# Kernel optimization log

Hardware: AMD Instinct MI355X
Metric: run time of the kernel (lower is better)

## Reference

```python
import jax, jax.numpy as jnp
import numpy as np

B, T, D = 256, 200, 32          # batch, time steps, input_size
H, PH, PREP = 512, 256, 16      # hidden_size, p_hidden, prep_hidden
COV, COVH, CLFH = 32, 128, 64   # cov_size, cov_hidden, classification_hidden
DT = 0.05                       # euler step size


def setup_inputs() -> dict:
    key = jax.random.key(0)
    ks = jax.random.split(key, 32)
    n = lambda k, shape, s=0.02: (s * jax.random.normal(k, shape)).astype(jnp.float32)
    inp = {}
    inp["cov"] = jax.random.normal(ks[0], (B, COV), dtype=jnp.float32)
    inp["X"] = jax.random.normal(ks[1], (T, B, D), dtype=jnp.float32)
    inp["M"] = (jax.random.uniform(ks[2], (T, B, D)) < 0.3).astype(jnp.float32)
    # covariates_mapping: Linear(COV,COVH) -> ReLU -> Linear(COVH,H) -> Tanh
    inp["Wc1"] = n(ks[3], (COVH, COV), 0.1); inp["bc1"] = jnp.full((COVH,), 0.05, jnp.float32)
    inp["Wc2"] = n(ks[4], (H, COVH), 0.1);   inp["bc2"] = jnp.full((H,), 0.05, jnp.float32)
    # GRUODECell: three bias-free Linear(H,H)
    inp["Whr"] = n(ks[5], (H, H), 0.05)
    inp["Whz"] = n(ks[6], (H, H), 0.05)
    inp["Whh"] = n(ks[7], (H, H), 0.05)
    # log_normal_dist: Linear(H,PH) -> ReLU -> Linear(PH, 2D)
    inp["Wp1"] = n(ks[8], (PH, H), 0.05);  inp["bp1"] = jnp.full((PH,), 0.05, jnp.float32)
    inp["Wp2"] = n(ks[9], (2 * D, PH), 0.05); inp["bp2"] = jnp.full((2 * D,), 0.05, jnp.float32)
    # GRUObsCell prep params
    std = np.sqrt(2.0 / (4 + PREP))
    inp["w_prep"] = (std * jax.random.normal(ks[10], (D, 4, PREP))).astype(jnp.float32)
    inp["bias_prep"] = jnp.full((D, PREP), 0.1, jnp.float32)
    # torch GRUCell(PREP*D, H): gates ordered (r, z, n)
    inp["W_ih"] = n(ks[11], (3 * H, PREP * D), 0.05)
    inp["W_hh"] = n(ks[12], (3 * H, H), 0.05)
    inp["b_ih"] = jnp.zeros((3 * H,), jnp.float32)
    inp["b_hh"] = jnp.zeros((3 * H,), jnp.float32)
    # classifier: Linear(H,CLFH) -> ReLU -> Linear(CLFH,1)
    inp["Wclf1"] = n(ks[13], (CLFH, H), 0.05); inp["bclf1"] = jnp.full((CLFH,), 0.05, jnp.float32)
    inp["Wclf2"] = n(ks[14], (1, CLFH), 0.05); inp["bclf2"] = jnp.full((1,), 0.05, jnp.float32)
    return inp


def reference(cov, X, M, Wc1, bc1, Wc2, bc2, Whr, Whz, Whh, Wp1, bp1, Wp2, bp2,
              w_prep, bias_prep, W_ih, W_hh, b_ih, b_hh, Wclf1, bclf1, Wclf2, bclf2):
    # initial hidden state from covariates
    h0 = jnp.tanh(jax.nn.relu(cov @ Wc1.T + bc1) @ Wc2.T + bc2)  # [B,H]

    def step(h, inp):
        Xt, Mt = inp  # [B,D], [B,D]
        # autonomous GRU-ODE euler step (impute=False -> zero input x)
        r = jax.nn.sigmoid(h @ Whr.T)
        z = jax.nn.sigmoid(h @ Whz.T)
        u = jnp.tanh((r * h) @ Whh.T)
        h = h + DT * (1.0 - z) * (u - h)
        # log-normal observation distribution from hidden state
        p = jax.nn.relu(h @ Wp1.T + bp1) @ Wp2.T + bp2  # [B,2D]
        mean, logvar = jnp.split(p, 2, axis=1)
        sigma = jnp.exp(0.5 * logvar)
        err = (Xt - mean) / sigma
        # per-feature preprocessing: [B,D,4] x [D,4,PREP] -> [B,D,PREP]
        stacked = jnp.stack([Xt, mean, logvar, err], axis=2)
        gi = jax.nn.relu(jnp.einsum('bdf,dfp->bdp', stacked, w_prep) + bias_prep)
        gi = (gi * Mt[:, :, None]).reshape(Xt.shape[0], -1)  # [B, D*PREP]
        # torch GRUCell update (gates r,z,n)
        gx = gi @ W_ih.T + b_ih
        gh = h @ W_hh.T + b_hh
        xr, xz, xn = jnp.split(gx, 3, axis=1)
        hr, hz, hn = jnp.split(gh, 3, axis=1)
        rg = jax.nn.sigmoid(xr + hr)
        zg = jax.nn.sigmoid(xz + hz)
        ng = jnp.tanh(xn + rg * hn)
        h_new = (1.0 - zg) * ng + zg * h
        # scatter-style update: only rows with at least one observation (i_obs)
        obs = (jnp.sum(Mt, axis=1) > 0.0)[:, None]
        h = jnp.where(obs, h_new, h)
        return h, h

    _, h_path = jax.lax.scan(step, h0, (X, M))  # [T,B,H]
    preds = jax.nn.relu(h_path @ Wclf1.T + bclf1) @ Wclf2.T + bclf2  # [T,B,1]
    return preds
```

## Files before the change

### kernel.cpp

```cpp
#include <hip/hip_runtime.h>
#include <hip/hip_bf16.h>

constexpr int Bn = 256, Tn = 200, Dn = 32, Hn = 512, PHn = 256, PREPn = 16;
constexpr int COVn = 32, COVHn = 128, CLFHn = 64;
constexpr float DTc = 0.05f;
constexpr int NT = 512;

constexpr int CSTR = 32;
constexpr int NLINES = 64;

typedef _Float16 h2v __attribute__((ext_vector_type(2)));
typedef _Float16 f16x8 __attribute__((ext_vector_type(8)));
typedef float f32x4 __attribute__((ext_vector_type(4)));

constexpr int PK_WP1   = 0;
constexpr int PK_WP2   = 131072;
constexpr int PK_WCLF1 = 147456;
constexpr int PK_TOTAL = 180224;

constexpr size_t WS_ACT = 393216;
constexpr size_t WS_OBS = 4587520;
constexpr size_t WS_BAR = 4591616;

__device__ __forceinline__ float sigmoidf(float x) { return 1.0f / (1.0f + __expf(-x)); }

__device__ __forceinline__ float fdot2(unsigned w, unsigned v, float acc) {
#if __has_builtin(__builtin_amdgcn_fdot2)
  return __builtin_amdgcn_fdot2(__builtin_bit_cast(h2v, w),
                                __builtin_bit_cast(h2v, v), acc, false);
#else
  h2v a = __builtin_bit_cast(h2v, w), b = __builtin_bit_cast(h2v, v);
  return acc + (float)a.x * (float)b.x + (float)a.y * (float)b.y;
#endif
}
__device__ __forceinline__ float dotq(uint4 w, uint4 h, float acc) {
  acc = fdot2(w.x, h.x, acc); acc = fdot2(w.y, h.y, acc);
  acc = fdot2(w.z, h.z, acc); acc = fdot2(w.w, h.w, acc);
  return acc;
}
__device__ __forceinline__ unsigned pack2(float a, float b) {
  h2v h; h.x = (_Float16)a; h.y = (_Float16)b;
  return __builtin_bit_cast(unsigned, h);
}

__device__ __forceinline__ void cohS(unsigned long long* p, unsigned long long v) {
  __hip_atomic_store(p, v, __ATOMIC_RELAXED, __HIP_MEMORY_SCOPE_SYSTEM);
}
__device__ __forceinline__ void cohSf(float* p, float v) {
  __hip_atomic_store(p, v, __ATOMIC_RELAXED, __HIP_MEMORY_SCOPE_SYSTEM);
}

__device__ __forceinline__ void bar_arrive(unsigned* ctrs, int rg) {
  __syncthreads();
  if (threadIdx.x == 0)
    __hip_atomic_fetch_add(&ctrs[rg * CSTR], 1u,
                           __ATOMIC_RELAXED, __HIP_MEMORY_SCOPE_AGENT);
}
__device__ __forceinline__ void bar_wait(unsigned* ctrs, int rg, unsigned& ep) {
  ep += 1;
  const unsigned target = ep * 64u;
  if (threadIdx.x == 0) {
    const unsigned* myc = &ctrs[rg * CSTR];
    while (__hip_atomic_load(myc, __ATOMIC_RELAXED, __HIP_MEMORY_SCOPE_AGENT) < target)
      __builtin_amdgcn_s_sleep(1);
  }
  __syncthreads();
}

struct PrepArgs { const float *Wp1, *Wp2, *Wclf1; _Float16* dst; unsigned* bar; };

__global__ void prep_pack_kernel(PrepArgs a) {
  const int idx = blockIdx.x * 256 + threadIdx.x;
  if (idx < NLINES * CSTR) a.bar[idx] = 0u;
  if (idx >= PK_TOTAL) return;
  int off, N, K; const float* src;
  if      (idx < PK_WP2)   { off = PK_WP1;   N = 256; K = 512; src = a.Wp1; }
  else if (idx < PK_WCLF1) { off = PK_WP2;   N = 64;  K = 256; src = a.Wp2; }
  else                     { off = PK_WCLF1; N = 64;  K = 512; src = a.Wclf1; }
  const int li = idx - off, e = li & 7, t2 = li >> 3, j = t2 % N, k8 = t2 / N;
  a.dst[idx] = (_Float16)src[(size_t)j * K + k8 * 8 + e];
}

struct CoopArgs {
  const float *cov, *X, *M;
  const float *Wc1, *bc1, *Wc2, *bc2;
  const float *Whr, *Whz, *Whh;
  const float *bp1, *bp2;
  const float *w_prep, *bias_prep;
  const float *W_ih, *W_hh, *b_ih, *b_hh;
  const float *bclf1, *Wclf2, *bclf2;
  const uint4 *Wp1Q, *Wp2Q, *Wclf1Q;
  char* act;
  float* obs;
  unsigned* bar;
  float* out;
};

__global__ __launch_bounds__(NT)
void gruode_coop(CoopArgs a) {
  const int bid = blockIdx.x, tid = threadIdx.x;
  const int cg = bid >> 2, rg = bid & 3;
  const int g = rg * 64 + cg;
  const int c_loc = tid >> 6, r_loc = tid & 63;
  const int c = cg * 8 + c_loc;
  const int lane = tid & 63, wv = tid >> 6;
  const int mt = wv & 3, kh = wv >> 2;
  const int pp4 = wv >> 2;
  const int rgofs = rg * 64;

  __shared__ __align__(16) uint4 Wrz16[64 * 17];
  __shared__ __align__(16) uint4 Wxrz16[64 * 17];
  __shared__ __align__(16) uint4 Whrz16[64 * 17];
  __shared__ __align__(16) uint4 Whh8[64 * 9];
  __shared__ __align__(16) uint4 Wxn8[64 * 9];
  __shared__ __align__(16) uint4 Whn8[64 * 9];
  __shared__ __align__(16) uint4 stageQ[64 * 64];
  __shared__ float redQ[2][64][17];
  __shared__ __align__(16) uint4 hrowQ[64];
  __shared__ __align__(16) uint4 qrowQ[32];
  __shared__ __align__(8)  _Float16 outH[512];
  __shared__ __align__(8)  _Float16 giH[512];
  __shared__ float bp1L[PHn], bp2L[2 * Dn], pL[2 * Dn];
  __shared__ float xrowL[Dn], mrowL[Dn];
  __shared__ float bclfL[CLFHn], wclf2L[CLFHn], bgL[48];
  __shared__ float obsL[64];

  unsigned long long* outU = (unsigned long long*)outH;
  unsigned long long* giU  = (unsigned long long*)giH;

  auto slabp = [&](int arr, int buf) -> uint4* {
    return (uint4*)(a.act + ((size_t)(arr * 4 + buf) << 18));
  };

  float hfull;
  {
    float* covF = (float*)redQ;
    float* midF = (float*)stageQ;
    for (int i = tid; i < 64 * 32; i += NT)
      covF[i] = a.cov[(size_t)rgofs * COVn + i];
    __syncthreads();
    for (int i = tid; i < 64 * 128; i += NT) {
      const int rr = i >> 7, m = i & 127;
      float acc = a.bc1[m];
      #pragma unroll 8
      for (int k = 0; k < COVn; ++k) acc += covF[rr * 32 + k] * a.Wc1[m * COVn + k];
      midF[i] = fmaxf(acc, 0.0f);
    }
    __syncthreads();
    {
      float acc = a.bc2[c];
      const float* w2 = a.Wc2 + (size_t)c * COVHn;
      #pragma unroll 4
      for (int k = 0; k < COVHn; ++k) acc += midF[r_loc * 128 + k] * w2[k];
      hfull = tanhf(acc);
      outH[r_loc * 8 + c_loc] = (_Float16)hfull;
    }
    __syncthreads();
    unsigned long long* hA3u = (unsigned long long*)slabp(0, 3);
    const size_t oub0 = (size_t)(cg * 256 + rgofs) * 2;
    if (tid < 128) cohS(&hA3u[oub0 + tid], outU[tid]);
    __syncthreads();
  }

  for (int nfo = tid; nfo < 4608; nfo += NT) {
    int li; const float* srow; uint4* dst; int phys;
    if (nfo < 3072) {
      li = nfo & 1023; const int seg = nfo >> 10;
      const int n = li >> 6, q = li & 63;
      const int col = cg * 8 + (n & 7);
      if (seg == 0)      { srow = (n < 8 ? a.Whr : a.Whz) + (size_t)col * Hn; dst = Wrz16; }
      else if (seg == 1) { srow = a.W_ih + (size_t)((n < 8 ? 0 : Hn) + col) * Hn; dst = Wxrz16; }
      else               { srow = a.W_hh + (size_t)((n < 8 ? 0 : Hn) + col) * Hn; dst = Whrz16; }
      phys = q * 17 + n;
      const float* s8 = srow + q * 8;
      uint4 u;
      u.x = pack2(s8[0], s8[1]); u.y = pack2(s8[2], s8[3]);
      u.z = pack2(s8[4], s8[5]); u.w = pack2(s8[6], s8[7]);
      dst[phys] = u;
    } else {
      li = (nfo - 3072) & 511; const int seg = (nfo - 3072) >> 9;
      const int n = li >> 6, q = li & 63;
      const int col = cg * 8 + n;
      if (seg == 0)      { srow = a.Whh + (size_t)col * Hn; dst = Whh8; }
      else if (seg == 1) { srow = a.W_ih + (size_t)(2 * Hn + col) * Hn; dst = Wxn8; }
      else               { srow = a.W_hh + (size_t)(2 * Hn + col) * Hn; dst = Whn8; }
      phys = q * 9 + n;
      const float* s8 = srow + q * 8;
      uint4 u;
      u.x = pack2(s8[0], s8[1]); u.y = pack2(s8[2], s8[3]);
      u.z = pack2(s8[4], s8[5]); u.w = pack2(s8[6], s8[7]);
      dst[phys] = u;
    }
  }
  if (tid < PHn)    bp1L[tid] = a.bp1[tid];
  if (tid < 2 * Dn) bp2L[tid] = a.bp2[tid];
  if (tid < CLFHn)  { bclfL[tid] = a.bclf1[tid]; wclf2L[tid] = a.Wclf2[tid]; }
  if (tid < 48) {
    const int cl = tid / 6, rem = tid % 6, gate = rem >> 1, s = rem & 1;
    const int j = gate * Hn + cg * 8 + cl;
    bgL[tid] = s ? a.b_hh[j] : a.b_ih[j];
  }
  if (tid >= 64 && tid < 96)        xrowL[tid - 64] = a.X[(size_t)g * Dn + (tid - 64)];
  else if (tid >= 96 && tid < 128)  mrowL[tid - 96] = a.M[(size_t)g * Dn + (tid - 96)];
  const float bclf2r = a.bclf2[0];

  unsigned ep = 0;
  bar_arrive(a.bar, rg); bar_wait(a.bar, rg, ep);

  float zz = 0.f, hbc = 0.f;
  const size_t oub = (size_t)(cg * 256 + rgofs) * 2;

  auto stage_fill = [&](const uint4* A) {
    #pragma unroll
    for (int i = 0; i < 8; ++i) {
      const int idx = tid + i * NT;
      stageQ[idx] = A[(size_t)(idx >> 6) * 256 + rgofs + (idx & 63)];
    }
  };

  auto ldA = [&](int ks) -> f16x8 {
    return __builtin_bit_cast(f16x8,
        stageQ[(4 * ks + (lane >> 4)) * 64 + mt * 16 + (lane & 15)]);
  };
  auto mma_wide = [&](const uint4* Bw) -> f32x4 {
    f32x4 acc = {0.f, 0.f, 0.f, 0.f};
    const int n = lane & 15, l4 = lane >> 4;
    #pragma unroll
    for (int i = 0; i < 8; ++i) {
      const int ks = kh * 8 + i;
      const f16x8 bv = __builtin_bit_cast(f16x8, Bw[(ks * 4 + l4) * 17 + n]);
      acc = __builtin_amdgcn_mfma_f32_16x16x32_f16(ldA(ks), bv, acc, 0, 0, 0);
    }
    return acc;
  };
  auto mma_half = [&](const uint4* Bw) -> f32x4 {
    f32x4 acc = {0.f, 0.f, 0.f, 0.f};
    const int n = lane & 15, l4 = lane >> 4;
    #pragma unroll
    for (int i = 0; i < 8; ++i) {
      const int ks = kh * 8 + i;
      uint4 ub = {0u, 0u, 0u, 0u};
      if (n < 8) ub = Bw[(ks * 4 + l4) * 9 + n];
      acc = __builtin_amdgcn_mfma_f32_16x16x32_f16(ldA(ks), __builtin_bit_cast(f16x8, ub),
                                                   acc, 0, 0, 0);
    }
    return acc;
  };
  auto redw = [&](f32x4 acc) {
    const int col = lane & 15, r0 = mt * 16 + ((lane >> 4) << 2);
    #pragma unroll
    for (int j = 0; j < 4; ++j) redQ[kh][r0 + j][col] = acc[j];
  };
  auto mma_p4 = [&](const uint4* Bw16, const uint4* Bw9) {
    f32x4 acc = {0.f, 0.f, 0.f, 0.f};
    const int n = lane & 15, l4 = lane >> 4;
    #pragma unroll
    for (int ks = 0; ks < 16; ++ks) {
      uint4 ub = {0u, 0u, 0u, 0u};
      if (pp4 == 0)      ub = Bw16[(ks * 4 + l4) * 17 + n];
      else if (n < 8)    ub = Bw9[(ks * 4 + l4) * 9 + n];
      acc = __builtin_amdgcn_mfma_f32_16x16x32_f16(ldA(ks), __builtin_bit_cast(f16x8, ub),
                                                   acc, 0, 0, 0);
    }
    const int col = lane & 15, r0 = mt * 16 + ((lane >> 4) << 2);
    #pragma unroll
    for (int j = 0; j < 4; ++j) redQ[pp4][r0 + j][col] = acc[j];
  };

  auto do_clf = [&](const uint4* hAbase, int tout) {
    if (tid < CLFHn) {
      hrowQ[tid] = hAbase[(size_t)tid * 256 + g];
      float acc = bclfL[tid];
      #pragma unroll 8
      for (int q = 0; q < Hn / 8; ++q) acc = dotq(a.Wclf1Q[q * CLFHn + tid], hrowQ[q], acc);
      float cc = fmaxf(acc, 0.0f) * wclf2L[tid];
      #pragma unroll
      for (int o = 32; o; o >>= 1) cc += __shfl_down(cc, o, 64);
      if (tid == 0) a.out[tout * Bn + g] = cc + bclf2r;
    }
  };

  for (int t = 0; t < Tn; ++t) {
    if ((t & 3) == 0) __builtin_amdgcn_fence(__ATOMIC_ACQUIRE, "agent");

    const int bs = t & 3, bp = (t + 3) & 3;
    const uint4* hA_prev = slabp(0, bp);
    uint4* rh_cur = slabp(1, bs);
    uint4* hB_cur = slabp(2, bs);
    uint4* gi_cur = slabp(3, bs);
    uint4* hA_cur = slabp(0, bs);
    float* obs_cur = a.obs + bs * 256;

    stage_fill(hA_prev);
    __syncthreads();
    redw(mma_wide(Wrz16));
    __syncthreads();
    {
      const float sr = redQ[0][r_loc][c_loc]     + redQ[1][r_loc][c_loc];
      const float sz = redQ[0][r_loc][c_loc + 8] + redQ[1][r_loc][c_loc + 8];
      const float rr = sigmoidf(sr);
      zz = sigmoidf(sz);
      outH[r_loc * 8 + c_loc] = (_Float16)(rr * hfull);
    }
    __syncthreads();
    if (tid < 128) cohS(((unsigned long long*)rh_cur) + oub + tid, outU[tid]);
    bar_arrive(a.bar, rg);
    if (t > 0) do_clf(hA_prev, t - 1);
    bar_wait(a.bar, rg, ep);

    stage_fill(rh_cur);
    __syncthreads();
    redw(mma_half(Whh8));
    __syncthreads();
    {
      const float su = redQ[0][r_loc][c_loc] + redQ[1][r_loc][c_loc];
      const float u = tanhf(su);
      hbc = hfull + DTc * (1.0f - zz) * (u - hfull);
      outH[r_loc * 8 + c_loc] = (_Float16)hbc;
    }
    __syncthreads();
    if (tid < 128) cohS(((unsigned long long*)hB_cur) + oub + tid, outU[tid]);
    bar_arrive(a.bar, rg);
    bar_wait(a.bar, rg, ep);

    if (tid < 64) hrowQ[tid] = hB_cur[(size_t)tid * 256 + g];
    __syncthreads();
    if (tid < PHn) {
      float a0 = bp1L[tid], a1 = 0.f;
      #pragma unroll 8
      for (int q = 0; q < Hn / 8; q += 2) {
        a0 = dotq(a.Wp1Q[q * PHn + tid], hrowQ[q], a0);
        a1 = dotq(a.Wp1Q[(q + 1) * PHn + tid], hrowQ[q + 1], a1);
      }
      ((_Float16*)qrowQ)[tid] = (_Float16)fmaxf(a0 + a1, 0.0f);
    }
    __syncthreads();
    if (tid < 2 * Dn) {
      float acc = bp2L[tid];
      #pragma unroll 4
      for (int q = 0; q < PHn / 8; ++q)
        acc = dotq(a.Wp2Q[q * (2 * Dn) + tid], qrowQ[q], acc);
      pL[tid] = acc;
    }
    __syncthreads();
    {
      const int d = tid >> 4, pp = tid & 15;
      const float xv   = xrowL[d];
      const float mean = pL[d];
      const float logv = pL[Dn + d];
      const float err  = (xv - mean) * __expf(-0.5f * logv);
      float acc = a.bias_prep[d * PREPn + pp];
      acc += xv   * a.w_prep[(d * 4 + 0) * PREPn + pp];
      acc += mean * a.w_prep[(d * 4 + 1) * PREPn + pp];
      acc += logv * a.w_prep[(d * 4 + 2) * PREPn + pp];
      acc += err  * a.w_prep[(d * 4 + 3) * PREPn + pp];
      giH[tid] = (_Float16)(fmaxf(acc, 0.0f) * mrowL[d]);
      if (tid < 32) {
        const unsigned long long bb = __ballot(mrowL[tid] > 0.0f);
        if (tid == 0) cohSf(&obs_cur[g], bb ? 1.0f : 0.0f);
      }
    }
    __syncthreads();
    if (tid < 128)
      cohS(((unsigned long long*)gi_cur) + (size_t)(tid >> 1) * 512 + g * 2 + (tid & 1), giU[tid]);
    bar_arrive(a.bar, rg);

    stage_fill(hB_cur);
    __syncthreads();
    mma_p4(Whrz16, Whn8);
    __syncthreads();
    const float hr = redQ[0][r_loc][c_loc];
    const float hz = redQ[0][r_loc][c_loc + 8];
    const float hn = redQ[1][r_loc][c_loc];
    bar_wait(a.bar, rg, ep);

    stage_fill(gi_cur);
    if (tid < 64) obsL[tid] = obs_cur[rgofs + tid];
    __syncthreads();
    mma_p4(Wxrz16, Wxn8);
    __syncthreads();
    {
      const float xr = redQ[0][r_loc][c_loc];
      const float xz = redQ[0][r_loc][c_loc + 8];
      const float xn = redQ[1][r_loc][c_loc];
      const float rgg = sigmoidf(xr + hr + bgL[c_loc * 6 + 0] + bgL[c_loc * 6 + 1]);
      const float zgg = sigmoidf(xz + hz + bgL[c_loc * 6 + 2] + bgL[c_loc * 6 + 3]);
      const float ng  = tanhf(xn + bgL[c_loc * 6 + 4] + rgg * (hn + bgL[c_loc * 6 + 5]));
      hfull = (obsL[r_loc] > 0.0f) ? ((1.0f - zgg) * ng + zgg * hbc) : hbc;
      outH[r_loc * 8 + c_loc] = (_Float16)hfull;
    }
    __syncthreads();
    if (tid < 128) cohS(((unsigned long long*)hA_cur) + oub + tid, outU[tid]);
    bar_arrive(a.bar, rg);
    if (t + 1 < Tn) {
      if (tid >= 64 && tid < 96)        xrowL[tid - 64] = a.X[((size_t)(t + 1) * Bn + g) * Dn + (tid - 64)];
      else if (tid >= 96 && tid < 128)  mrowL[tid - 96] = a.M[((size_t)(t + 1) * Bn + g) * Dn + (tid - 96)];
    }
    bar_wait(a.bar, rg, ep);
  }

  do_clf(slabp(0, (Tn - 1) & 3), Tn - 1);
}

extern "C" void kernel_launch(void* const* d_in, const int* in_sizes, int n_in,
                              void* d_out, int out_size, void* d_ws, size_t ws_size,
                              hipStream_t stream) {
  char* ws = (char*)d_ws;

  CoopArgs a;
  a.cov  = (const float*)d_in[0];
  a.X    = (const float*)d_in[1];
  a.M    = (const float*)d_in[2];
  a.Wc1  = (const float*)d_in[3];  a.bc1 = (const float*)d_in[4];
  a.Wc2  = (const float*)d_in[5];  a.bc2 = (const float*)d_in[6];
  a.Whr  = (const float*)d_in[7];  a.Whz = (const float*)d_in[8];  a.Whh = (const float*)d_in[9];
  const float* Wp1 = (const float*)d_in[10]; a.bp1 = (const float*)d_in[11];
  const float* Wp2 = (const float*)d_in[12]; a.bp2 = (const float*)d_in[13];
  a.w_prep = (const float*)d_in[14]; a.bias_prep = (const float*)d_in[15];
  a.W_ih = (const float*)d_in[16]; a.W_hh = (const float*)d_in[17];
  a.b_ih = (const float*)d_in[18]; a.b_hh = (const float*)d_in[19];
  const float* Wclf1 = (const float*)d_in[20]; a.bclf1 = (const float*)d_in[21];
  a.Wclf2 = (const float*)d_in[22]; a.bclf2 = (const float*)d_in[23];

  _Float16* pk = (_Float16*)ws;
  a.Wp1Q   = (const uint4*)(pk + PK_WP1);
  a.Wp2Q   = (const uint4*)(pk + PK_WP2);
  a.Wclf1Q = (const uint4*)(pk + PK_WCLF1);
  a.act = ws + WS_ACT;
  a.obs = (float*)(ws + WS_OBS);
  a.bar = (unsigned*)(ws + WS_BAR);
  a.out = (float*)d_out;

  PrepArgs p;
  p.Wp1 = Wp1; p.Wp2 = Wp2; p.Wclf1 = Wclf1;
  p.dst = pk; p.bar = a.bar;
  prep_pack_kernel<<<(PK_TOTAL + 255) / 256, 256, 0, stream>>>(p);
  gruode_coop<<<Bn, NT, 0, stream>>>(a);
}
```

Baseline: 5.083 ms.

## Compute obs-cell prep redundantly per block with MFMA, dropping one grid barrier

```diff
diff --git a/kernel.cpp b/kernel.cpp
--- a/kernel.cpp
+++ b/kernel.cpp
@@ -7,7 +7,6 @@
 constexpr int NT = 512;
 
 constexpr int CSTR = 32;
-constexpr int NLINES = 64;
 
 typedef _Float16 h2v __attribute__((ext_vector_type(2)));
 typedef _Float16 f16x8 __attribute__((ext_vector_type(8)));
@@ -16,11 +15,11 @@
 constexpr int PK_WP1   = 0;
 constexpr int PK_WP2   = 131072;
 constexpr int PK_WCLF1 = 147456;
-constexpr int PK_TOTAL = 180224;
-
-constexpr size_t WS_ACT = 393216;
-constexpr size_t WS_OBS = 4587520;
-constexpr size_t WS_BAR = 4591616;
+constexpr int PK_WIH   = 180224;
+constexpr int PK_TOTAL = 966656;
+
+constexpr size_t WS_ACT = 1933312;
+constexpr size_t WS_BAR = 4292608;
 
 __device__ __forceinline__ float sigmoidf(float x) { return 1.0f / (1.0f + __expf(-x)); }
 
@@ -44,9 +43,6 @@
 }
 
 __device__ __forceinline__ void cohS(unsigned long long* p, unsigned long long v) {
-  __hip_atomic_store(p, v, __ATOMIC_RELAXED, __HIP_MEMORY_SCOPE_SYSTEM);
-}
-__device__ __forceinline__ void cohSf(float* p, float v) {
   __hip_atomic_store(p, v, __ATOMIC_RELAXED, __HIP_MEMORY_SCOPE_SYSTEM);
 }
 
@@ -67,18 +63,27 @@
   __syncthreads();
 }
 
-struct PrepArgs { const float *Wp1, *Wp2, *Wclf1; _Float16* dst; unsigned* bar; };
+struct PrepArgs { const float *Wp1, *Wp2, *Wclf1, *W_ih; _Float16* dst; unsigned* bar; };
 
 __global__ void prep_pack_kernel(PrepArgs a) {
   const int idx = blockIdx.x * 256 + threadIdx.x;
-  if (idx < NLINES * CSTR) a.bar[idx] = 0u;
+  if (idx < 4 * CSTR) a.bar[idx] = 0u;
   if (idx >= PK_TOTAL) return;
-  int off, N, K; const float* src;
-  if      (idx < PK_WP2)   { off = PK_WP1;   N = 256; K = 512; src = a.Wp1; }
-  else if (idx < PK_WCLF1) { off = PK_WP2;   N = 64;  K = 256; src = a.Wp2; }
-  else                     { off = PK_WCLF1; N = 64;  K = 512; src = a.Wclf1; }
-  const int li = idx - off, e = li & 7, t2 = li >> 3, j = t2 % N, k8 = t2 / N;
-  a.dst[idx] = (_Float16)src[(size_t)j * K + k8 * 8 + e];
+  if (idx < PK_WIH) {
+    int off, N, K; const float* src;
+    if      (idx < PK_WP2)   { off = PK_WP1;   N = 256; K = 512; src = a.Wp1; }
+    else if (idx < PK_WCLF1) { off = PK_WP2;   N = 64;  K = 256; src = a.Wp2; }
+    else                     { off = PK_WCLF1; N = 64;  K = 512; src = a.Wclf1; }
+    const int li = idx - off, e = li & 7, t2 = li >> 3, j = t2 % N, k8 = t2 / N;
+    a.dst[idx] = (_Float16)src[(size_t)j * K + k8 * 8 + e];
+  } else {
+    const int li = idx - PK_WIH;
+    const int e = li & 7, t2 = li >> 3;
+    const int col = t2 % 24, u = t2 / 24;
+    const int k8 = u & 63, cg = u >> 6;
+    const int gate = col >> 3;
+    a.dst[idx] = (_Float16)a.W_ih[(size_t)(gate * Hn + cg * 8 + (col & 7)) * Hn + k8 * 8 + e];
+  }
 }
 
 struct CoopArgs {
@@ -89,9 +94,8 @@
   const float *w_prep, *bias_prep;
   const float *W_ih, *W_hh, *b_ih, *b_hh;
   const float *bclf1, *Wclf2, *bclf2;
-  const uint4 *Wp1Q, *Wp2Q, *Wclf1Q;
+  const uint4 *Wp1Q, *Wp2Q, *Wclf1Q, *WihQ;
   char* act;
-  float* obs;
   unsigned* bar;
   float* out;
 };
@@ -104,32 +108,31 @@
   const int c_loc = tid >> 6, r_loc = tid & 63;
   const int c = cg * 8 + c_loc;
   const int lane = tid & 63, wv = tid >> 6;
-  const int mt = wv & 3, kh = wv >> 2;
-  const int pp4 = wv >> 2;
+  const int mtw = wv & 3, kh = wv >> 2;
+  const int n16 = lane & 15, l4 = lane >> 4;
   const int rgofs = rg * 64;
 
-  __shared__ __align__(16) uint4 Wrz16[64 * 17];
-  __shared__ __align__(16) uint4 Wxrz16[64 * 17];
-  __shared__ __align__(16) uint4 Whrz16[64 * 17];
-  __shared__ __align__(16) uint4 Whh8[64 * 9];
-  __shared__ __align__(16) uint4 Wxn8[64 * 9];
-  __shared__ __align__(16) uint4 Whn8[64 * 9];
+  __shared__ __align__(16) uint4 Wrz16L[64 * 16];
+  __shared__ __align__(16) uint4 Whrz16L[64 * 16];
+  __shared__ __align__(16) uint4 Whh8L[64 * 8];
+  __shared__ __align__(16) uint4 Whn8L[64 * 8];
   __shared__ __align__(16) uint4 stageQ[64 * 64];
   __shared__ float redQ[2][64][17];
-  __shared__ __align__(16) uint4 hrowQ[64];
-  __shared__ __align__(16) uint4 qrowQ[32];
-  __shared__ __align__(8)  _Float16 outH[512];
-  __shared__ __align__(8)  _Float16 giH[512];
-  __shared__ float bp1L[PHn], bp2L[2 * Dn], pL[2 * Dn];
-  __shared__ float xrowL[Dn], mrowL[Dn];
+  __shared__ _Float16 pT[64][66];
+  __shared__ float xrowT[32][64];
+  __shared__ unsigned mmaskL[64];
+  __shared__ float wprepL[Dn * 4 * PREPn];
+  __shared__ float bprepL[Dn * PREPn];
+  __shared__ float bp1L[PHn], bp2L[2 * Dn];
   __shared__ float bclfL[CLFHn], wclf2L[CLFHn], bgL[48];
-  __shared__ float obsL[64];
-
-  unsigned long long* outU = (unsigned long long*)outH;
-  unsigned long long* giU  = (unsigned long long*)giH;
+  __shared__ __align__(16) uint4 sh64[64];
+
+  _Float16* stageH = (_Float16*)stageQ;
+  unsigned long long* outU = (unsigned long long*)sh64;
+  _Float16* outH = (_Float16*)sh64;
 
   auto slabp = [&](int arr, int buf) -> uint4* {
-    return (uint4*)(a.act + ((size_t)(arr * 4 + buf) << 18));
+    return (uint4*)(a.act + ((size_t)(arr * 3 + buf) << 18));
   };
 
   float hfull;
@@ -153,45 +156,44 @@
       #pragma unroll 4
       for (int k = 0; k < COVHn; ++k) acc += midF[r_loc * 128 + k] * w2[k];
       hfull = tanhf(acc);
-      outH[r_loc * 8 + c_loc] = (_Float16)hfull;
-    }
-    __syncthreads();
-    unsigned long long* hA3u = (unsigned long long*)slabp(0, 3);
+    }
+    __syncthreads();
+    outH[r_loc * 8 + c_loc] = (_Float16)hfull;
+    __syncthreads();
+    unsigned long long* hA2u = (unsigned long long*)slabp(0, 2);
     const size_t oub0 = (size_t)(cg * 256 + rgofs) * 2;
-    if (tid < 128) cohS(&hA3u[oub0 + tid], outU[tid]);
+    if (tid < 128) cohS(&hA2u[oub0 + tid], outU[tid]);
     __syncthreads();
   }
 
-  for (int nfo = tid; nfo < 4608; nfo += NT) {
-    int li; const float* srow; uint4* dst; int phys;
-    if (nfo < 3072) {
-      li = nfo & 1023; const int seg = nfo >> 10;
-      const int n = li >> 6, q = li & 63;
-      const int col = cg * 8 + (n & 7);
-      if (seg == 0)      { srow = (n < 8 ? a.Whr : a.Whz) + (size_t)col * Hn; dst = Wrz16; }
-      else if (seg == 1) { srow = a.W_ih + (size_t)((n < 8 ? 0 : Hn) + col) * Hn; dst = Wxrz16; }
-      else               { srow = a.W_hh + (size_t)((n < 8 ? 0 : Hn) + col) * Hn; dst = Whrz16; }
-      phys = q * 17 + n;
-      const float* s8 = srow + q * 8;
-      uint4 u;
-      u.x = pack2(s8[0], s8[1]); u.y = pack2(s8[2], s8[3]);
-      u.z = pack2(s8[4], s8[5]); u.w = pack2(s8[6], s8[7]);
-      dst[phys] = u;
+  for (int nfo = tid; nfo < 3072; nfo += NT) {
+    const float* srow; uint4* dst; int q, phys;
+    if (nfo < 1024) {
+      q = nfo & 63; const int n = nfo >> 6;
+      srow = (n < 8 ? a.Whr + (size_t)(cg * 8 + n) * Hn
+                    : a.Whz + (size_t)(cg * 8 + n - 8) * Hn);
+      dst = Wrz16L; phys = q * 16 + n;
+    } else if (nfo < 2048) {
+      const int li = nfo - 1024; q = li & 63; const int n = li >> 6;
+      srow = a.W_hh + (size_t)((n < 8 ? 0 : Hn) + cg * 8 + (n & 7)) * Hn;
+      dst = Whrz16L; phys = q * 16 + n;
+    } else if (nfo < 2560) {
+      const int li = nfo - 2048; q = li & 63; const int n = li >> 6;
+      srow = a.Whh + (size_t)(cg * 8 + n) * Hn;
+      dst = Whh8L; phys = q * 8 + n;
     } else {
-      li = (nfo - 3072) & 511; const int seg = (nfo - 3072) >> 9;
-      const int n = li >> 6, q = li & 63;
-      const int col = cg * 8 + n;
-      if (seg == 0)      { srow = a.Whh + (size_t)col * Hn; dst = Whh8; }
-      else if (seg == 1) { srow = a.W_ih + (size_t)(2 * Hn + col) * Hn; dst = Wxn8; }
-      else               { srow = a.W_hh + (size_t)(2 * Hn + col) * Hn; dst = Whn8; }
-      phys = q * 9 + n;
-      const float* s8 = srow + q * 8;
-      uint4 u;
-      u.x = pack2(s8[0], s8[1]); u.y = pack2(s8[2], s8[3]);
-      u.z = pack2(s8[4], s8[5]); u.w = pack2(s8[6], s8[7]);
-      dst[phys] = u;
-    }
+      const int li = nfo - 2560; q = li & 63; const int n = li >> 6;
+      srow = a.W_hh + (size_t)(2 * Hn + cg * 8 + n) * Hn;
+      dst = Whn8L; phys = q * 8 + n;
+    }
+    const float* s8 = srow + q * 8;
+    uint4 u;
+    u.x = pack2(s8[0], s8[1]); u.y = pack2(s8[2], s8[3]);
+    u.z = pack2(s8[4], s8[5]); u.w = pack2(s8[6], s8[7]);
+    dst[phys] = u;
   }
+  for (int i = tid; i < Dn * 4 * PREPn; i += NT) wprepL[i] = a.w_prep[i];
+  if (tid < Dn * PREPn) bprepL[tid] = a.bias_prep[tid];
   if (tid < PHn)    bp1L[tid] = a.bp1[tid];
   if (tid < 2 * Dn) bp2L[tid] = a.bp2[tid];
   if (tid < CLFHn)  { bclfL[tid] = a.bclf1[tid]; wclf2L[tid] = a.Wclf2[tid]; }
@@ -200,9 +202,23 @@
     const int j = gate * Hn + cg * 8 + cl;
     bgL[tid] = s ? a.b_hh[j] : a.b_ih[j];
   }
-  if (tid >= 64 && tid < 96)        xrowL[tid - 64] = a.X[(size_t)g * Dn + (tid - 64)];
-  else if (tid >= 96 && tid < 128)  mrowL[tid - 96] = a.M[(size_t)g * Dn + (tid - 96)];
   const float bclf2r = a.bclf2[0];
+  const uint4* WihB = a.WihQ + (size_t)cg * 64 * 24;
+
+  auto loadXM = [&](int t) {
+    const float* Xs = a.X + ((size_t)t * Bn + rgofs) * Dn;
+    const float* Ms = a.M + ((size_t)t * Bn + rgofs) * Dn;
+    #pragma unroll
+    for (int i = 0; i < 4; ++i) {
+      const int idx = tid + i * NT;
+      xrowT[idx & 31][idx >> 5] = Xs[idx];
+      const float m = Ms[idx];
+      const unsigned long long b = __ballot(m > 0.0f);
+      if ((lane & 31) == 0)
+        mmaskL[idx >> 5] = (unsigned)(lane < 32 ? b : (b >> 32));
+    }
+  };
+  loadXM(0);
 
   unsigned ep = 0;
   bar_arrive(a.bar, rg); bar_wait(a.bar, rg, ep);
@@ -217,62 +233,16 @@
       stageQ[idx] = A[(size_t)(idx >> 6) * 256 + rgofs + (idx & 63)];
     }
   };
-
-  auto ldA = [&](int ks) -> f16x8 {
-    return __builtin_bit_cast(f16x8,
-        stageQ[(4 * ks + (lane >> 4)) * 64 + mt * 16 + (lane & 15)]);
+  auto ldA = [&](int mt, int ks) -> f16x8 {
+    return __builtin_bit_cast(f16x8, stageQ[(4 * ks + l4) * 64 + mt * 16 + n16]);
   };
-  auto mma_wide = [&](const uint4* Bw) -> f32x4 {
-    f32x4 acc = {0.f, 0.f, 0.f, 0.f};
-    const int n = lane & 15, l4 = lane >> 4;
-    #pragma unroll
-    for (int i = 0; i < 8; ++i) {
-      const int ks = kh * 8 + i;
-      const f16x8 bv = __builtin_bit_cast(f16x8, Bw[(ks * 4 + l4) * 17 + n]);
-      acc = __builtin_amdgcn_mfma_f32_16x16x32_f16(ldA(ks), bv, acc, 0, 0, 0);
-    }
-    return acc;
-  };
-  auto mma_half = [&](const uint4* Bw) -> f32x4 {
-    f32x4 acc = {0.f, 0.f, 0.f, 0.f};
-    const int n = lane & 15, l4 = lane >> 4;
-    #pragma unroll
-    for (int i = 0; i < 8; ++i) {
-      const int ks = kh * 8 + i;
-      uint4 ub = {0u, 0u, 0u, 0u};
-      if (n < 8) ub = Bw[(ks * 4 + l4) * 9 + n];
-      acc = __builtin_amdgcn_mfma_f32_16x16x32_f16(ldA(ks), __builtin_bit_cast(f16x8, ub),
-                                                   acc, 0, 0, 0);
-    }
-    return acc;
-  };
-  auto redw = [&](f32x4 acc) {
-    const int col = lane & 15, r0 = mt * 16 + ((lane >> 4) << 2);
-    #pragma unroll
-    for (int j = 0; j < 4; ++j) redQ[kh][r0 + j][col] = acc[j];
-  };
-  auto mma_p4 = [&](const uint4* Bw16, const uint4* Bw9) {
-    f32x4 acc = {0.f, 0.f, 0.f, 0.f};
-    const int n = lane & 15, l4 = lane >> 4;
-    #pragma unroll
-    for (int ks = 0; ks < 16; ++ks) {
-      uint4 ub = {0u, 0u, 0u, 0u};
-      if (pp4 == 0)      ub = Bw16[(ks * 4 + l4) * 17 + n];
-      else if (n < 8)    ub = Bw9[(ks * 4 + l4) * 9 + n];
-      acc = __builtin_amdgcn_mfma_f32_16x16x32_f16(ldA(ks), __builtin_bit_cast(f16x8, ub),
-                                                   acc, 0, 0, 0);
-    }
-    const int col = lane & 15, r0 = mt * 16 + ((lane >> 4) << 2);
-    #pragma unroll
-    for (int j = 0; j < 4; ++j) redQ[pp4][r0 + j][col] = acc[j];
-  };
-
-  auto do_clf = [&](const uint4* hAbase, int tout) {
+
+  auto do_clf = [&](int tout) {
     if (tid < CLFHn) {
-      hrowQ[tid] = hAbase[(size_t)tid * 256 + g];
+      sh64[tid] = stageQ[tid * 64 + cg];
       float acc = bclfL[tid];
       #pragma unroll 8
-      for (int q = 0; q < Hn / 8; ++q) acc = dotq(a.Wclf1Q[q * CLFHn + tid], hrowQ[q], acc);
+      for (int q = 0; q < Hn / 8; ++q) acc = dotq(a.Wclf1Q[q * CLFHn + tid], sh64[q], acc);
       float cc = fmaxf(acc, 0.0f) * wclf2L[tid];
       #pragma unroll
       for (int o = 32; o; o >>= 1) cc += __shfl_down(cc, o, 64);
@@ -280,37 +250,58 @@
     }
   };
 
+  int bs = 0;
   for (int t = 0; t < Tn; ++t) {
-    if ((t & 3) == 0) __builtin_amdgcn_fence(__ATOMIC_ACQUIRE, "agent");
-
-    const int bs = t & 3, bp = (t + 3) & 3;
+    if (bs == 0) __builtin_amdgcn_fence(__ATOMIC_ACQUIRE, "agent");
+    const int bp = (bs + 2 >= 3) ? bs - 1 : bs + 2;
     const uint4* hA_prev = slabp(0, bp);
     uint4* rh_cur = slabp(1, bs);
     uint4* hB_cur = slabp(2, bs);
-    uint4* gi_cur = slabp(3, bs);
     uint4* hA_cur = slabp(0, bs);
-    float* obs_cur = a.obs + bs * 256;
 
     stage_fill(hA_prev);
     __syncthreads();
-    redw(mma_wide(Wrz16));
+    {
+      f32x4 acc = {0.f, 0.f, 0.f, 0.f};
+      #pragma unroll
+      for (int i = 0; i < 8; ++i) {
+        const int ks = kh * 8 + i;
+        const f16x8 bv = __builtin_bit_cast(f16x8, Wrz16L[(ks * 4 + l4) * 16 + n16]);
+        acc = __builtin_amdgcn_mfma_f32_16x16x32_f16(ldA(mtw, ks), bv, acc, 0, 0, 0);
+      }
+      const int r0 = mtw * 16 + (l4 << 2);
+      #pragma unroll
+      for (int j = 0; j < 4; ++j) redQ[kh][r0 + j][n16] = acc[j];
+    }
     __syncthreads();
     {
       const float sr = redQ[0][r_loc][c_loc]     + redQ[1][r_loc][c_loc];
       const float sz = redQ[0][r_loc][c_loc + 8] + redQ[1][r_loc][c_loc + 8];
-      const float rr = sigmoidf(sr);
       zz = sigmoidf(sz);
-      outH[r_loc * 8 + c_loc] = (_Float16)(rr * hfull);
+      outH[r_loc * 8 + c_loc] = (_Float16)(sigmoidf(sr) * hfull);
     }
     __syncthreads();
     if (tid < 128) cohS(((unsigned long long*)rh_cur) + oub + tid, outU[tid]);
     bar_arrive(a.bar, rg);
-    if (t > 0) do_clf(hA_prev, t - 1);
+    if (t > 0) do_clf(t - 1);
     bar_wait(a.bar, rg, ep);
 
     stage_fill(rh_cur);
     __syncthreads();
-    redw(mma_half(Whh8));
+    {
+      f32x4 acc = {0.f, 0.f, 0.f, 0.f};
+      #pragma unroll
+      for (int i = 0; i < 8; ++i) {
+        const int ks = kh * 8 + i;
+        uint4 ub = {0u, 0u, 0u, 0u};
+        if (n16 < 8) ub = Whh8L[(ks * 4 + l4) * 8 + n16];
+        acc = __builtin_amdgcn_mfma_f32_16x16x32_f16(ldA(mtw, ks),
+                __builtin_bit_cast(f16x8, ub), acc, 0, 0, 0);
+      }
+      const int r0 = mtw * 16 + (l4 << 2);
+      #pragma unroll
+      for (int j = 0; j < 4; ++j) redQ[kh][r0 + j][n16] = acc[j];
+    }
     __syncthreads();
     {
       const float su = redQ[0][r_loc][c_loc] + redQ[1][r_loc][c_loc];
@@ -321,63 +312,136 @@
     __syncthreads();
     if (tid < 128) cohS(((unsigned long long*)hB_cur) + oub + tid, outU[tid]);
     bar_arrive(a.bar, rg);
+    loadXM(t);
     bar_wait(a.bar, rg, ep);
 
-    if (tid < 64) hrowQ[tid] = hB_cur[(size_t)tid * 256 + g];
-    __syncthreads();
-    if (tid < PHn) {
-      float a0 = bp1L[tid], a1 = 0.f;
-      #pragma unroll 8
-      for (int q = 0; q < Hn / 8; q += 2) {
-        a0 = dotq(a.Wp1Q[q * PHn + tid], hrowQ[q], a0);
-        a1 = dotq(a.Wp1Q[(q + 1) * PHn + tid], hrowQ[q + 1], a1);
-      }
-      ((_Float16*)qrowQ)[tid] = (_Float16)fmaxf(a0 + a1, 0.0f);
-    }
-    __syncthreads();
-    if (tid < 2 * Dn) {
-      float acc = bp2L[tid];
-      #pragma unroll 4
-      for (int q = 0; q < PHn / 8; ++q)
-        acc = dotq(a.Wp2Q[q * (2 * Dn) + tid], qrowQ[q], acc);
-      pL[tid] = acc;
-    }
-    __syncthreads();
-    {
-      const int d = tid >> 4, pp = tid & 15;
-      const float xv   = xrowL[d];
-      const float mean = pL[d];
-      const float logv = pL[Dn + d];
-      const float err  = (xv - mean) * __expf(-0.5f * logv);
-      float acc = a.bias_prep[d * PREPn + pp];
-      acc += xv   * a.w_prep[(d * 4 + 0) * PREPn + pp];
-      acc += mean * a.w_prep[(d * 4 + 1) * PREPn + pp];
-      acc += logv * a.w_prep[(d * 4 + 2) * PREPn + pp];
-      acc += err  * a.w_prep[(d * 4 + 3) * PREPn + pp];
-      giH[tid] = (_Float16)(fmaxf(acc, 0.0f) * mrowL[d]);
-      if (tid < 32) {
-        const unsigned long long bb = __ballot(mrowL[tid] > 0.0f);
-        if (tid == 0) cohSf(&obs_cur[g], bb ? 1.0f : 0.0f);
-      }
-    }
-    __syncthreads();
-    if (tid < 128)
-      cohS(((unsigned long long*)gi_cur) + (size_t)(tid >> 1) * 512 + g * 2 + (tid & 1), giU[tid]);
-    bar_arrive(a.bar, rg);
-
     stage_fill(hB_cur);
     __syncthreads();
-    mma_p4(Whrz16, Whn8);
+    {
+      f32x4 acc = {0.f, 0.f, 0.f, 0.f};
+      #pragma unroll
+      for (int ks = 0; ks < 16; ++ks) {
+        uint4 ub = {0u, 0u, 0u, 0u};
+        if (kh == 0)        ub = Whrz16L[(ks * 4 + l4) * 16 + n16];
+        else if (n16 < 8)   ub = Whn8L[(ks * 4 + l4) * 8 + n16];
+        acc = __builtin_amdgcn_mfma_f32_16x16x32_f16(ldA(mtw, ks),
+                __builtin_bit_cast(f16x8, ub), acc, 0, 0, 0);
+      }
+      const int r0 = mtw * 16 + (l4 << 2);
+      #pragma unroll
+      for (int j = 0; j < 4; ++j) redQ[kh][r0 + j][n16] = acc[j];
+    }
     __syncthreads();
     const float hr = redQ[0][r_loc][c_loc];
     const float hz = redQ[0][r_loc][c_loc + 8];
     const float hn = redQ[1][r_loc][c_loc];
-    bar_wait(a.bar, rg, ep);
-
-    stage_fill(gi_cur);
-    if (tid < 64) obsL[tid] = obs_cur[rgofs + tid];
-    __syncthreads();
-    mma_p4(Wxrz16, Wxn8);
+
+    {
+      f32x4 qa[4][2];
+      #pragma unroll
+      for (int mt = 0; mt < 4; ++mt)
+        #pragma unroll
+        for (int h = 0; h < 2; ++h) {
+          const float b = bp1L[(wv * 2 + h) * 16 + n16];
+          qa[mt][h] = f32x4{b, b, b, b};
+        }
+      #pragma unroll 4
+      for (int ks = 0; ks < 16; ++ks) {
+        f16x8 A0 = ldA(0, ks), A1 = ldA(1, ks), A2 = ldA(2, ks), A3 = ldA(3, ks);
+        #pragma unroll
+        for (int h = 0; h < 2; ++h) {
+          const f16x8 bv = __builtin_bit_cast(f16x8,
+              a.Wp1Q[(ks * 4 + l4) * 256 + (wv * 2 + h) * 16 + n16]);
+          qa[0][h] = __builtin_amdgcn_mfma_f32_16x16x32_f16(A0, bv, qa[0][h], 0, 0, 0);
+          qa[1][h] = __builtin_amdgcn_mfma_f32_16x16x32_f16(A1, bv, qa[1][h], 0, 0, 0);
+          qa[2][h] = __builtin_amdgcn_mfma_f32_16x16x32_f16(A2, bv, qa[2][h], 0, 0, 0);
+          qa[3][h] = __builtin_amdgcn_mfma_f32_16x16x32_f16(A3, bv, qa[3][h], 0, 0, 0);
+        }
+      }
+      __syncthreads();
+      #pragma unroll
+      for (int mt = 0; mt < 4; ++mt)
+        #pragma unroll
+        for (int h = 0; h < 2; ++h) {
+          const int k = (wv * 2 + h) * 16 + n16;
+          #pragma unroll
+          for (int j = 0; j < 4; ++j) {
+            const int row = mt * 16 + l4 * 4 + j;
+            stageH[(k >> 3) * 512 + row * 8 + (k & 7)] =
+                (_Float16)fmaxf(qa[mt][h][j], 0.0f);
+          }
+        }
+      __syncthreads();
+    }
+
+    {
+      f32x4 pa[2];
+      #pragma unroll
+      for (int h = 0; h < 2; ++h) {
+        const float b = bp2L[(kh * 2 + h) * 16 + n16];
+        pa[h] = f32x4{b, b, b, b};
+      }
+      #pragma unroll
+      for (int ks = 0; ks < 8; ++ks) {
+        const f16x8 A = ldA(mtw, ks);
+        #pragma unroll
+        for (int h = 0; h < 2; ++h) {
+          const f16x8 bv = __builtin_bit_cast(f16x8,
+              a.Wp2Q[(ks * 4 + l4) * 64 + (kh * 2 + h) * 16 + n16]);
+          pa[h] = __builtin_amdgcn_mfma_f32_16x16x32_f16(A, bv, pa[h], 0, 0, 0);
+        }
+      }
+      __syncthreads();
+      #pragma unroll
+      for (int h = 0; h < 2; ++h)
+        #pragma unroll
+        for (int j = 0; j < 4; ++j)
+          pT[(kh * 2 + h) * 16 + n16][mtw * 16 + l4 * 4 + j] = (_Float16)pa[h][j];
+      __syncthreads();
+    }
+
+    {
+      #pragma unroll
+      for (int i = 0; i < 8; ++i) {
+        const int idx = tid + i * NT;
+        const int oct = idx >> 6, row = idx & 63;
+        const int d = oct >> 1, p0 = (oct & 1) * 8;
+        const float xv   = xrowT[d][row];
+        const float mean = (float)pT[d][row];
+        const float logv = (float)pT[32 + d][row];
+        const float err  = (xv - mean) * __expf(-0.5f * logv);
+        const float msk  = ((mmaskL[row] >> d) & 1u) ? 1.0f : 0.0f;
+        const float* wp = &wprepL[d * 4 * PREPn];
+        f16x8 g8;
+        #pragma unroll
+        for (int e = 0; e < 8; ++e) {
+          const int pp = p0 + e;
+          float acc = bprepL[d * PREPn + pp];
+          acc += xv   * wp[0 * PREPn + pp];
+          acc += mean * wp[1 * PREPn + pp];
+          acc += logv * wp[2 * PREPn + pp];
+          acc += err  * wp[3 * PREPn + pp];
+          g8[e] = (_Float16)(fmaxf(acc, 0.0f) * msk);
+        }
+        stageQ[idx] = __builtin_bit_cast(uint4, g8);
+      }
+      __syncthreads();
+    }
+
+    {
+      f32x4 acc = {0.f, 0.f, 0.f, 0.f};
+      #pragma unroll
+      for (int ks = 0; ks < 16; ++ks) {
+        uint4 ub = {0u, 0u, 0u, 0u};
+        if (kh == 0)        ub = WihB[(ks * 4 + l4) * 24 + n16];
+        else if (n16 < 8)   ub = WihB[(ks * 4 + l4) * 24 + 16 + n16];
+        acc = __builtin_amdgcn_mfma_f32_16x16x32_f16(ldA(mtw, ks),
+                __builtin_bit_cast(f16x8, ub), acc, 0, 0, 0);
+      }
+      const int r0 = mtw * 16 + (l4 << 2);
+      #pragma unroll
+      for (int j = 0; j < 4; ++j) redQ[kh][r0 + j][n16] = acc[j];
+    }
     __syncthreads();
     {
       const float xr = redQ[0][r_loc][c_loc];
@@ -386,20 +450,21 @@
       const float rgg = sigmoidf(xr + hr + bgL[c_loc * 6 + 0] + bgL[c_loc * 6 + 1]);
       const float zgg = sigmoidf(xz + hz + bgL[c_loc * 6 + 2] + bgL[c_loc * 6 + 3]);
       const float ng  = tanhf(xn + bgL[c_loc * 6 + 4] + rgg * (hn + bgL[c_loc * 6 + 5]));
-      hfull = (obsL[r_loc] > 0.0f) ? ((1.0f - zgg) * ng + zgg * hbc) : hbc;
+      hfull = (mmaskL[r_loc] != 0u) ? ((1.0f - zgg) * ng + zgg * hbc) : hbc;
       outH[r_loc * 8 + c_loc] = (_Float16)hfull;
     }
     __syncthreads();
     if (tid < 128) cohS(((unsigned long long*)hA_cur) + oub + tid, outU[tid]);
     bar_arrive(a.bar, rg);
-    if (t + 1 < Tn) {
-      if (tid >= 64 && tid < 96)        xrowL[tid - 64] = a.X[((size_t)(t + 1) * Bn + g) * Dn + (tid - 64)];
-      else if (tid >= 96 && tid < 128)  mrowL[tid - 96] = a.M[((size_t)(t + 1) * Bn + g) * Dn + (tid - 96)];
-    }
+    if (t + 1 < Tn) loadXM(t + 1);
     bar_wait(a.bar, rg, ep);
+
+    bs = (bs + 1 >= 3) ? 0 : bs + 1;
   }
 
-  do_clf(slabp(0, (Tn - 1) & 3), Tn - 1);
+  stage_fill(slabp(0, (Tn - 1) % 3));
+  __syncthreads();
+  do_clf(Tn - 1);
 }
 
 extern "C" void kernel_launch(void* const* d_in, const int* in_sizes, int n_in,
@@ -426,13 +491,13 @@
   a.Wp1Q   = (const uint4*)(pk + PK_WP1);
   a.Wp2Q   = (const uint4*)(pk + PK_WP2);
   a.Wclf1Q = (const uint4*)(pk + PK_WCLF1);
+  a.WihQ   = (const uint4*)(pk + PK_WIH);
   a.act = ws + WS_ACT;
-  a.obs = (float*)(ws + WS_OBS);
   a.bar = (unsigned*)(ws + WS_BAR);
   a.out = (float*)d_out;
 
   PrepArgs p;
-  p.Wp1 = Wp1; p.Wp2 = Wp2; p.Wclf1 = Wclf1;
+  p.Wp1 = Wp1; p.Wp2 = Wp2; p.Wclf1 = Wclf1; p.W_ih = a.W_ih;
   p.dst = pk; p.bar = a.bar;
   prep_pack_kernel<<<(PK_TOTAL + 255) / 256, 256, 0, stream>>>(p);
   gruode_coop<<<Bn, NT, 0, stream>>>(a);
```

New measurement: 7.682 ms. 51.1% more time.
